# Kernel tuning notes

Measured on AMD Instinct MI355X. Metric: run time of the kernel, lower is better.

## Reference

```python
import jax, jax.numpy as jnp
import numpy as np

NUM_CODES = 4096
EMBED_DIM = 64
BETA = 0.25


def setup_inputs() -> dict:
    key = jax.random.key(0)
    k1, k2 = jax.random.split(key)
    z = jax.random.normal(k1, (8, EMBED_DIM, 64, 64), dtype=jnp.float32)
    weight = jax.random.normal(k2, (NUM_CODES, EMBED_DIM), dtype=jnp.float32)
    return {"z": z, "weight": weight}


def reference(z, weight):
    # z: [B, C, H, W] -> [B, H, W, C]
    z_bhwc = jnp.moveaxis(z, 1, -1)
    z_flat = z_bhwc.reshape(-1, EMBED_DIM)  # [N, d]

    # squared-euclidean distances: ||z||^2 + ||w||^2 - 2 z.w  -> [N, num_codes]
    distance = (
        jnp.sum(z_flat ** 2, axis=1, keepdims=True)
        + jnp.sum(weight ** 2, axis=1)
        - 2.0 * jnp.einsum('bd,nd->bn', z_flat, weight)
    )
    encoding_indices = jnp.argmin(distance, axis=1)  # [N]

    # codebook lookup (gather)
    z_q = weight[encoding_indices].reshape(z_bhwc.shape)  # [B, H, W, C]

    encodings = jax.nn.one_hot(encoding_indices, NUM_CODES, dtype=z.dtype)  # [N, num_codes]
    avg_probs = jnp.mean(encodings, axis=0)
    tiny = 1e-10  # max(1e-10, finfo(fp32).tiny)
    perplexity = jnp.exp(-jnp.sum(avg_probs * jnp.log(avg_probs + tiny)))

    # commitment loss (z_q detached) — eval path, no EMA state update
    loss = BETA * jnp.mean((jax.lax.stop_gradient(z_q) - z_bhwc) ** 2)

    # straight-through estimator
    z_q = z_bhwc + jax.lax.stop_gradient(z_q - z_bhwc)
    z_q = jnp.moveaxis(z_q, -1, 1)  # back to [B, C, H, W]

    return z_q, loss, perplexity, encodings, encoding_indices
```

## Files before the change

### kernel.cpp

```cpp
#include <hip/hip_runtime.h>
#include <math.h>
#include <float.h>

#define ZQ_OFF   0
#define LOSS_OFF 2097152
#define PERP_OFF 2097153
#define ENC_OFF  2097154
#define IDX_OFF  136314882ULL
#define BETA     0.25f


__global__ void vq_wnorm(const float* __restrict__ w, float* __restrict__ wnorm) {
    int c = blockIdx.x * 256 + threadIdx.x;
    const float4* w4 = (const float4*)(w + ((size_t)c << 6));
    float s = 0.f;
    #pragma unroll
    for (int k = 0; k < 16; ++k) { float4 v = w4[k]; s += v.x*v.x + v.y*v.y + v.z*v.z + v.w*v.w; }
    wnorm[c] = s;
}

__global__ __launch_bounds__(256, 2) void vq_main(
    const float* __restrict__ z, const float* __restrict__ w,
    const float* __restrict__ wnorm, float* __restrict__ out,
    float* __restrict__ loss_ws, int* __restrict__ ticket, int* __restrict__ hist)
{
    __shared__ float zD[64][64];
    __shared__ float wl[256 * 36];
    __shared__ int   s_widx[64];
    __shared__ int   s_flag;

    const int tx   = threadIdx.x;
    const int tcol = tx & 31;
    const int trow = tx >> 5;
    const int base = blockIdx.x * 64;
    const int bb   = base >> 12;
    const int hh   = (base & 4095) >> 6;

    #pragma unroll
    for (int j = 0; j < 4; ++j) {
        int f4 = j * 256 + tx;
        int d  = f4 >> 4, w4i = f4 & 15;
        float4 v = *(const float4*)(z + (((size_t)bb * 64 + d) * 64 + hh) * 64 + w4i * 4);
        *(float4*)&zD[d][w4i * 4] = v;
    }

    float best[8]; int bidx[8];
    #pragma unroll
    for (int i = 0; i < 8; ++i) { best[i] = FLT_MAX; bidx[i] = 0; }

    float* enc = out + ENC_OFF;

    for (int ch = 0; ch < 16; ++ch) {
        const int cbase = ch << 8;
        float wn[8];
        #pragma unroll
        for (int k = 0; k < 8; ++k) wn[k] = wnorm[cbase + tcol + 32 * k];

        float acc[8][8];
        #pragma unroll
        for (int i = 0; i < 8; ++i)
            #pragma unroll
            for (int k = 0; k < 8; ++k) acc[i][k] = 0.f;

        #pragma unroll
        for (int s = 0; s < 2; ++s) {
            __syncthreads();
            #pragma unroll
            for (int j = 0; j < 8; ++j) {
                int f4 = j * 256 + tx;
                int c  = f4 >> 3, q = f4 & 7;
                float4 v = ((const float4*)w)[(size_t)(cbase + c) * 16 + s * 8 + q];
                *(float4*)&wl[c * 36 + q * 4] = v;
            }
            #pragma unroll
            for (int j = 0; j < 16; ++j) {
                int f2 = ((ch * 2 + s) * 16 + j) * 256 + tx;
                int r  = f2 >> 11, c2 = f2 & 2047;
                *((float2*)(enc + ((size_t)(base + r) << 12)) + c2) = make_float2(0.f, 0.f);
            }
            __syncthreads();

            #pragma unroll
            for (int dg = 0; dg < 8; ++dg) {
                const int d0 = s * 32 + dg * 4;
                float4 zv0[4], zv1[4];
                #pragma unroll
                for (int e = 0; e < 4; ++e) {
                    zv0[e] = *(const float4*)&zD[d0 + e][trow * 8];
                    zv1[e] = *(const float4*)&zD[d0 + e][trow * 8 + 4];
                }
                float4 wv[8];
                #pragma unroll
                for (int k = 0; k < 8; ++k)
                    wv[k] = *(const float4*)&wl[(tcol + 32 * k) * 36 + dg * 4];
                #pragma unroll
                for (int k = 0; k < 8; ++k) {
                    #pragma unroll
                    for (int e = 0; e < 4; ++e) {
                        const float wf = (e == 0) ? wv[k].x : (e == 1) ? wv[k].y
                                        : (e == 2) ? wv[k].z : wv[k].w;
                        acc[0][k] = fmaf(zv0[e].x, wf, acc[0][k]);
                        acc[1][k] = fmaf(zv0[e].y, wf, acc[1][k]);
                        acc[2][k] = fmaf(zv0[e].z, wf, acc[2][k]);
                        acc[3][k] = fmaf(zv0[e].w, wf, acc[3][k]);
                        acc[4][k] = fmaf(zv1[e].x, wf, acc[4][k]);
                        acc[5][k] = fmaf(zv1[e].y, wf, acc[5][k]);
                        acc[6][k] = fmaf(zv1[e].z, wf, acc[6][k]);
                        acc[7][k] = fmaf(zv1[e].w, wf, acc[7][k]);
                    }
                }
            }
        }

        #pragma unroll
        for (int i = 0; i < 8; ++i) {
            #pragma unroll
            for (int k = 0; k < 8; ++k) {
                float sc = fmaf(-2.f, acc[i][k], wn[k]);
                if (sc < best[i]) { best[i] = sc; bidx[i] = cbase + tcol + 32 * k; }
            }
        }
    }

    __syncthreads();
    float2* red = (float2*)wl;
    #pragma unroll
    for (int i = 0; i < 8; ++i)
        red[(trow * 8 + i) * 32 + tcol] = make_float2(best[i], __int_as_float(bidx[i]));
    __syncthreads();

    if (tx < 64) {
        float b = FLT_MAX; int bi = 0x7fffffff;
        for (int c = 0; c < 32; ++c) {
            float2 v = red[tx * 32 + c];
            int vi = __float_as_int(v.y);
            if (v.x < b || (v.x == b && vi < bi)) { b = v.x; bi = vi; }
        }
        s_widx[tx] = bi;
        out[IDX_OFF + (size_t)(base + tx)] = (float)bi;
        atomicAdd(&hist[bi], 1);
        enc[((size_t)(base + tx) << 12) + bi] = 1.0f;
    }
    __syncthreads();

    {
        const int row = tx & 63;
        const int dg  = tx >> 6;
        const int wi  = s_widx[row];
        const float* qrow = w + ((size_t)wi << 6);
        float lsum = 0.f;
        #pragma unroll
        for (int dd = 0; dd < 16; ++dd) {
            int d = dg * 16 + dd;
            float q  = qrow[d];
            float zv = zD[d][row];
            float diff = q - zv;
            lsum += diff * diff;
            out[ZQ_OFF + (((size_t)bb * 64 + d) * 64 + hh) * 64 + row] = zv + (q - zv);
        }
        #pragma unroll
        for (int off = 32; off > 0; off >>= 1) lsum += __shfl_down(lsum, off, 64);
        if ((tx & 63) == 0) atomicAdd(loss_ws, lsum);
    }

    __syncthreads();
    if (tx == 0) {
        __threadfence();
        int old = atomicAdd(ticket, 1);
        s_flag = (old == 511) ? 1 : 0;
    }
    __syncthreads();
    if (s_flag) {
        __threadfence();
        float s = 0.f;
        #pragma unroll
        for (int j = 0; j < 16; ++j) {
            int c = tx + j * 256;
            int cnt = atomicAdd(&hist[c], 0);
            float p = (float)cnt * (1.f / 32768.f);
            s += p * logf(p + 1e-10f);
        }
        float* fr = wl;
        fr[tx] = s;
        __syncthreads();
        for (int off = 128; off > 0; off >>= 1) {
            if (tx < off) fr[tx] += fr[tx + off];
            __syncthreads();
        }
        if (tx == 0) {
            out[LOSS_OFF] = BETA * atomicAdd(loss_ws, 0.f) / 2097152.f;
            out[PERP_OFF] = expf(-fr[0]);
        }
    }
}

extern "C" void kernel_launch(void* const* d_in, const int* in_sizes, int n_in,
                              void* d_out, int out_size, void* d_ws, size_t ws_size,
                              hipStream_t stream)
{
    const float* z = (const float*)d_in[0];
    const float* w = (const float*)d_in[1];
    float* out     = (float*)d_out;
    float* loss_ws = (float*)d_ws;
    int*   ticket  = (int*)((char*)d_ws + 4);
    int*   hist    = (int*)((char*)d_ws + 16);
    float* wnorm   = (float*)((char*)d_ws + 16400);

    hipMemsetAsync(d_ws, 0, 16 + 4096 * sizeof(int), stream);
    vq_wnorm<<<16, 256, 0, stream>>>(w, wnorm);
    vq_main<<<512, 256, 0, stream>>>(z, w, wnorm, out, loss_ws, ticket, hist);
}
```

Measured before the change: 737.3 us.

## Compute VQ distances with split-bf16 MFMA and register-staged double buffering

Replaces the FP32 FMA distance GEMM with bf16 MFMA 16x16x32 instructions. Operands are split into three bf16 parts (high, mid, low) and six cross products are accumulated to keep near-FP32 accuracy. A prep kernel pre-splits the codebook. Codebook chunks are staged through registers into LDS one chunk ahead, and the argmin reduction uses wave shuffles instead of an LDS pass. The enc zero-fill is still interleaved and occupancy is raised to 3 blocks per CU. The risk is argmin ties or near-ties flipping, since the reduced-precision products are not exactly FP32.

```diff
diff --git a/kernel.cpp b/kernel.cpp
--- a/kernel.cpp
+++ b/kernel.cpp
@@ -10,6 +10,25 @@
 #define BETA     0.25f
 
 
+typedef __attribute__((ext_vector_type(8))) short short8;
+typedef __attribute__((ext_vector_type(4))) float f32x4;
+
+#define MFMA16(a, b, c) __builtin_amdgcn_mfma_f32_16x16x32_bf16(a, b, c, 0, 0, 0)
+
+__device__ __forceinline__ float bf16_rn(float v, unsigned short* h) {
+    unsigned u = __float_as_uint(v);
+    unsigned r = (u + 0x7fffu + ((u >> 16) & 1u)) & 0xffff0000u;
+    *h = (unsigned short)(r >> 16);
+    return __uint_as_float(r);
+}
+__device__ __forceinline__ void split3(float v, unsigned short* h, unsigned short* m, unsigned short* l) {
+    float hf = bf16_rn(v, h);
+    float r1 = v - hf;
+    float mf = bf16_rn(r1, m);
+    float r2 = r1 - mf;
+    bf16_rn(r2, l);
+}
+
 __global__ void vq_wnorm(const float* __restrict__ w, float* __restrict__ wnorm) {
     int c = blockIdx.x * 256 + threadIdx.x;
     const float4* w4 = (const float4*)(w + ((size_t)c << 6));
@@ -19,19 +38,36 @@
     wnorm[c] = s;
 }
 
-__global__ __launch_bounds__(256, 2) void vq_main(
+__global__ void vq_prep(const float* __restrict__ w, unsigned short* __restrict__ w3) {
+    int t = blockIdx.x * 256 + threadIdx.x;
+    int code = t >> 4, d0 = (t & 15) << 2;
+    float4 v = *(const float4*)(w + ((size_t)code << 6) + d0);
+    float vv[4] = {v.x, v.y, v.z, v.w};
+    unsigned short h[4], m[4], l[4];
+    #pragma unroll
+    for (int e = 0; e < 4; ++e) split3(vv[e], &h[e], &m[e], &l[e]);
+    size_t b = (size_t)code * 192 + d0;
+    *(ushort4*)(w3 + b)       = make_ushort4(h[0], h[1], h[2], h[3]);
+    *(ushort4*)(w3 + b + 64)  = make_ushort4(m[0], m[1], m[2], m[3]);
+    *(ushort4*)(w3 + b + 128) = make_ushort4(l[0], l[1], l[2], l[3]);
+}
+
+__global__ __launch_bounds__(256, 3) void vq_main(
     const float* __restrict__ z, const float* __restrict__ w,
-    const float* __restrict__ wnorm, float* __restrict__ out,
+    const float* __restrict__ wnorm, const unsigned short* __restrict__ w3,
+    float* __restrict__ out,
     float* __restrict__ loss_ws, int* __restrict__ ticket, int* __restrict__ hist)
 {
     __shared__ float zD[64][64];
-    __shared__ float wl[256 * 36];
-    __shared__ int   s_widx[64];
-    __shared__ int   s_flag;
+    __shared__ __align__(16) char wl[64 * 3 * 144];
+    __shared__ int s_widx[64];
+    __shared__ int s_flag;
 
     const int tx   = threadIdx.x;
-    const int tcol = tx & 31;
-    const int trow = tx >> 5;
+    const int lane = tx & 63;
+    const int wv   = tx >> 6;
+    const int lcol = lane & 15;
+    const int lkq  = lane >> 4;
     const int base = blockIdx.x * 64;
     const int bb   = base >> 12;
     const int hh   = (base & 4095) >> 6;
@@ -44,102 +80,122 @@
         *(float4*)&zD[d][w4i * 4] = v;
     }
 
-    float best[8]; int bidx[8];
-    #pragma unroll
-    for (int i = 0; i < 8; ++i) { best[i] = FLT_MAX; bidx[i] = 0; }
+    const char* w3b = (const char*)w3;
+    const int cL = tx >> 2, q = tx & 3;
+    const int tb = cL * 384 + q * 96;
+
+    float4 rA[6], rB[6];
+    #pragma unroll
+    for (int j = 0; j < 6; ++j) rA[j] = *(const float4*)(w3b + tb + j * 16);
+
+    __syncthreads();
+
+    short8 aH[2], aM[2], aL[2];
+    #pragma unroll
+    for (int s = 0; s < 2; ++s)
+        #pragma unroll
+        for (int j = 0; j < 8; ++j) {
+            float v = zD[s * 32 + lkq * 8 + j][wv * 16 + lcol];
+            unsigned short h, m, l;
+            split3(v, &h, &m, &l);
+            aH[s][j] = (short)h; aM[s][j] = (short)m; aL[s][j] = (short)l;
+        }
+
+    float best[4]; int bidx[4];
+    #pragma unroll
+    for (int r = 0; r < 4; ++r) { best[r] = FLT_MAX; bidx[r] = 0; }
 
     float* enc = out + ENC_OFF;
 
-    for (int ch = 0; ch < 16; ++ch) {
-        const int cbase = ch << 8;
-        float wn[8];
-        #pragma unroll
-        for (int k = 0; k < 8; ++k) wn[k] = wnorm[cbase + tcol + 32 * k];
-
-        float acc[8][8];
-        #pragma unroll
-        for (int i = 0; i < 8; ++i)
-            #pragma unroll
-            for (int k = 0; k < 8; ++k) acc[i][k] = 0.f;
-
-        #pragma unroll
-        for (int s = 0; s < 2; ++s) {
-            __syncthreads();
-            #pragma unroll
-            for (int j = 0; j < 8; ++j) {
-                int f4 = j * 256 + tx;
-                int c  = f4 >> 3, q = f4 & 7;
-                float4 v = ((const float4*)w)[(size_t)(cbase + c) * 16 + s * 8 + q];
-                *(float4*)&wl[c * 36 + q * 4] = v;
-            }
-            #pragma unroll
-            for (int j = 0; j < 16; ++j) {
-                int f2 = ((ch * 2 + s) * 16 + j) * 256 + tx;
-                int r  = f2 >> 11, c2 = f2 & 2047;
-                *((float2*)(enc + ((size_t)(base + r) << 12)) + c2) = make_float2(0.f, 0.f);
-            }
-            __syncthreads();
-
-            #pragma unroll
-            for (int dg = 0; dg < 8; ++dg) {
-                const int d0 = s * 32 + dg * 4;
-                float4 zv0[4], zv1[4];
-                #pragma unroll
-                for (int e = 0; e < 4; ++e) {
-                    zv0[e] = *(const float4*)&zD[d0 + e][trow * 8];
-                    zv1[e] = *(const float4*)&zD[d0 + e][trow * 8 + 4];
-                }
-                float4 wv[8];
-                #pragma unroll
-                for (int k = 0; k < 8; ++k)
-                    wv[k] = *(const float4*)&wl[(tcol + 32 * k) * 36 + dg * 4];
-                #pragma unroll
-                for (int k = 0; k < 8; ++k) {
-                    #pragma unroll
-                    for (int e = 0; e < 4; ++e) {
-                        const float wf = (e == 0) ? wv[k].x : (e == 1) ? wv[k].y
-                                        : (e == 2) ? wv[k].z : wv[k].w;
-                        acc[0][k] = fmaf(zv0[e].x, wf, acc[0][k]);
-                        acc[1][k] = fmaf(zv0[e].y, wf, acc[1][k]);
-                        acc[2][k] = fmaf(zv0[e].z, wf, acc[2][k]);
-                        acc[3][k] = fmaf(zv0[e].w, wf, acc[3][k]);
-                        acc[4][k] = fmaf(zv1[e].x, wf, acc[4][k]);
-                        acc[5][k] = fmaf(zv1[e].y, wf, acc[5][k]);
-                        acc[6][k] = fmaf(zv1[e].z, wf, acc[6][k]);
-                        acc[7][k] = fmaf(zv1[e].w, wf, acc[7][k]);
-                    }
-                }
-            }
-        }
-
-        #pragma unroll
-        for (int i = 0; i < 8; ++i) {
-            #pragma unroll
-            for (int k = 0; k < 8; ++k) {
-                float sc = fmaf(-2.f, acc[i][k], wn[k]);
-                if (sc < best[i]) { best[i] = sc; bidx[i] = cbase + tcol + 32 * k; }
-            }
-        }
-    }
-
-    __syncthreads();
-    float2* red = (float2*)wl;
-    #pragma unroll
-    for (int i = 0; i < 8; ++i)
-        red[(trow * 8 + i) * 32 + tcol] = make_float2(best[i], __int_as_float(bidx[i]));
-    __syncthreads();
-
-    if (tx < 64) {
-        float b = FLT_MAX; int bi = 0x7fffffff;
-        for (int c = 0; c < 32; ++c) {
-            float2 v = red[tx * 32 + c];
-            int vi = __float_as_int(v.y);
-            if (v.x < b || (v.x == b && vi < bi)) { b = v.x; bi = vi; }
-        }
-        s_widx[tx] = bi;
-        out[IDX_OFF + (size_t)(base + tx)] = (float)bi;
-        atomicAdd(&hist[bi], 1);
-        enc[((size_t)(base + tx) << 12) + bi] = 1.0f;
+#define STAGE_WRITE(R) { \
+    _Pragma("unroll") \
+    for (int j = 0; j < 6; ++j) { \
+        int o = q * 96 + j * 16; \
+        *(float4*)&wl[(cL * 3 + (o >> 7)) * 144 + (o & 127)] = R[j]; \
+    } }
+
+#define STAGE_LOAD(R, CH) { \
+    const char* sp = w3b + (size_t)(CH) * 24576 + tb; \
+    _Pragma("unroll") \
+    for (int j = 0; j < 6; ++j) R[j] = *(const float4*)(sp + j * 16); }
+
+#define ZFILL(CH) { \
+    _Pragma("unroll") \
+    for (int j = 0; j < 8; ++j) { \
+        int f2 = ((CH) * 8 + j) * 256 + tx; \
+        int rr = f2 >> 11, cc2 = f2 & 2047; \
+        *((float2*)(enc + ((size_t)(base + rr) << 12)) + cc2) = make_float2(0.f, 0.f); \
+    } }
+
+#define COMPUTE(CH) { \
+    const int cbase = (CH) << 6; \
+    float wnv[4]; \
+    _Pragma("unroll") \
+    for (int t = 0; t < 4; ++t) wnv[t] = wnorm[cbase + t * 16 + lcol]; \
+    _Pragma("unroll 2") \
+    for (int t = 0; t < 4; ++t) { \
+        const int clocal = t * 16 + lcol; \
+        const char* bp = &wl[clocal * 432 + lkq * 16]; \
+        short8 bH0 = *(const short8*)(bp); \
+        short8 bH1 = *(const short8*)(bp + 64); \
+        short8 bM0 = *(const short8*)(bp + 144); \
+        short8 bM1 = *(const short8*)(bp + 208); \
+        short8 bL0 = *(const short8*)(bp + 288); \
+        short8 bL1 = *(const short8*)(bp + 352); \
+        f32x4 c0 = {0.f, 0.f, 0.f, 0.f}, c1 = {0.f, 0.f, 0.f, 0.f}, c2 = {0.f, 0.f, 0.f, 0.f}; \
+        c0 = MFMA16(aH[0], bH0, c0); c0 = MFMA16(aH[1], bH1, c0); \
+        c1 = MFMA16(aH[0], bM0, c1); c1 = MFMA16(aH[1], bM1, c1); \
+        c1 = MFMA16(aM[0], bH0, c1); c1 = MFMA16(aM[1], bH1, c1); \
+        c2 = MFMA16(aM[0], bM0, c2); c2 = MFMA16(aM[1], bM1, c2); \
+        c2 = MFMA16(aH[0], bL0, c2); c2 = MFMA16(aH[1], bL1, c2); \
+        c2 = MFMA16(aL[0], bH0, c2); c2 = MFMA16(aL[1], bH1, c2); \
+        _Pragma("unroll") \
+        for (int r = 0; r < 4; ++r) { \
+            float sdot = (c0[r] + c1[r]) + c2[r]; \
+            float dd = fmaf(-2.f, sdot, wnv[t]); \
+            if (dd < best[r]) { best[r] = dd; bidx[r] = cbase + clocal; } \
+        } \
+    } }
+
+    #pragma unroll 1
+    for (int cc = 0; cc < 32; ++cc) {
+        const int ch0 = cc * 2, ch1 = ch0 + 1;
+        __syncthreads();
+        STAGE_WRITE(rA);
+        __syncthreads();
+        STAGE_LOAD(rB, ch1);
+        ZFILL(ch0);
+        COMPUTE(ch0);
+        __syncthreads();
+        STAGE_WRITE(rB);
+        __syncthreads();
+        { const int nx = (ch1 + 1) & 63; STAGE_LOAD(rA, nx); }
+        ZFILL(ch1);
+        COMPUTE(ch1);
+    }
+
+    __syncthreads();
+
+    #pragma unroll
+    for (int mm = 1; mm < 16; mm <<= 1) {
+        #pragma unroll
+        for (int r = 0; r < 4; ++r) {
+            float ob = __shfl_xor(best[r], mm, 64);
+            int   oi = __shfl_xor(bidx[r], mm, 64);
+            if (ob < best[r] || (ob == best[r] && oi < bidx[r])) { best[r] = ob; bidx[r] = oi; }
+        }
+    }
+
+    if (lcol == 0) {
+        const int rowb = wv * 16 + lkq * 4;
+        #pragma unroll
+        for (int r = 0; r < 4; ++r) {
+            int row = rowb + r, bi = bidx[r];
+            s_widx[row] = bi;
+            out[IDX_OFF + (size_t)(base + row)] = (float)bi;
+            atomicAdd(&hist[bi], 1);
+            enc[((size_t)(base + row) << 12) + bi] = 1.0f;
+        }
     }
     __syncthreads();
 
@@ -152,11 +208,11 @@
         #pragma unroll
         for (int dd = 0; dd < 16; ++dd) {
             int d = dg * 16 + dd;
-            float q  = qrow[d];
+            float qv = qrow[d];
             float zv = zD[d][row];
-            float diff = q - zv;
+            float diff = qv - zv;
             lsum += diff * diff;
-            out[ZQ_OFF + (((size_t)bb * 64 + d) * 64 + hh) * 64 + row] = zv + (q - zv);
+            out[ZQ_OFF + (((size_t)bb * 64 + d) * 64 + hh) * 64 + row] = zv + (qv - zv);
         }
         #pragma unroll
         for (int off = 32; off > 0; off >>= 1) lsum += __shfl_down(lsum, off, 64);
@@ -180,7 +236,7 @@
             float p = (float)cnt * (1.f / 32768.f);
             s += p * logf(p + 1e-10f);
         }
-        float* fr = wl;
+        float* fr = (float*)wl;
         fr[tx] = s;
         __syncthreads();
         for (int off = 128; off > 0; off >>= 1) {
@@ -192,6 +248,10 @@
             out[PERP_OFF] = expf(-fr[0]);
         }
     }
+#undef STAGE_WRITE
+#undef STAGE_LOAD
+#undef ZFILL
+#undef COMPUTE
 }
 
 extern "C" void kernel_launch(void* const* d_in, const int* in_sizes, int n_in,
@@ -205,8 +265,11 @@
     int*   ticket  = (int*)((char*)d_ws + 4);
     int*   hist    = (int*)((char*)d_ws + 16);
     float* wnorm   = (float*)((char*)d_ws + 16400);
+    unsigned short* w3 = (unsigned short*)((char*)d_ws + 32800);
+    (void)ws_size; (void)in_sizes; (void)n_in; (void)out_size;
 
     hipMemsetAsync(d_ws, 0, 16 + 4096 * sizeof(int), stream);
     vq_wnorm<<<16, 256, 0, stream>>>(w, wnorm);
-    vq_main<<<512, 256, 0, stream>>>(z, w, wnorm, out, loss_ws, ticket, hist);
-}
+    vq_prep<<<256, 256, 0, stream>>>(w, w3);
+    vq_main<<<512, 256, 0, stream>>>(z, w, wnorm, w3, out, loss_ws, ticket, hist);
+}
```

After: 789.9 us. 1.07x slower.
